# Kernel optimization log

Hardware: AMD Instinct MI355X
Metric: run time of the kernel (lower is better)

## Reference

```python
import jax, jax.numpy as jnp
import numpy as np

N_NODES = 100000
N_EDGES = 2000000
EPS = 1e-8


def setup_inputs() -> dict:
    key = jax.random.key(0)
    k1, k2 = jax.random.split(key)
    node_positions = jax.random.normal(k1, (1, N_NODES, 2), dtype=jnp.float32) * 10.0
    adjacency = jnp.zeros((1, 1, 1), dtype=jnp.float32)  # unused by this axiom
    edge_index = jax.random.randint(k2, (2, N_EDGES), 0, N_NODES, dtype=jnp.int32)
    return {"node_positions": node_positions, "adjacency": adjacency, "edge_index": edge_index}


def reference(node_positions, adjacency, edge_index):
    """OrthogonalIntegrityAxiom loss.

    Mathematically identical to enumerating all intra-node edge pairs (i<j)
    and averaging cos^2(theta)*(1-cos^2(theta)) = dot^2 - dot^4 over pairs.
    Uses the moment identity: per node n with incident unit directions d_i,
      sum_{i,j} (d_i.d_j)^2 = ||sum_i d_i (x) d_i||_F^2
      sum_{i,j} (d_i.d_j)^4 = ||sum_i d_i^{(x)4}||_F^2
    Diagonal (i=j) terms equal 1 in both sums and cancel in the difference,
    so sum_{i<j} (dot^2 - dot^4) = (S2_n - S4_n)/2.
    """
    pos = node_positions.reshape(-1, 2)                      # (N, 2)
    n_total = pos.shape[0]
    src, dst = edge_index[0], edge_index[1]
    d = pos[dst] - pos[src]                                  # (E, 2)
    d = d / jnp.maximum(jnp.linalg.norm(d, axis=-1, keepdims=True), EPS)

    # Each edge is incident to both endpoints -> 2E (node, direction) pairs.
    nodes = jnp.concatenate([src, dst])                      # (2E,)
    dirs = jnp.concatenate([d, d], axis=0)                   # (2E, 2)

    o2 = (dirs[:, :, None] * dirs[:, None, :]).reshape(-1, 4)    # d (x) d, (2E, 4)
    o4 = (o2[:, :, None] * o2[:, None, :]).reshape(-1, 16)       # d^{(x)4}, (2E, 16)

    M = jax.ops.segment_sum(o2, nodes, num_segments=n_total)     # (N, 4)
    T = jax.ops.segment_sum(o4, nodes, num_segments=n_total)     # (N, 16)
    deg = jax.ops.segment_sum(jnp.ones_like(dirs[:, 0]), nodes, num_segments=n_total)

    S2 = jnp.sum(M * M, axis=-1)   # per-node sum_{i,j} (d_i.d_j)^2
    S4 = jnp.sum(T * T, axis=-1)   # per-node sum_{i,j} (d_i.d_j)^4

    pair_loss_sum = 0.5 * jnp.sum(S2 - S4)
    n_pairs = 0.5 * jnp.sum(deg * (deg - 1.0))
    loss = pair_loss_sum / jnp.maximum(n_pairs, 1.0)
    return loss
```

## Files before the change

kernel.cpp:

```cpp
#include <hip/hip_runtime.h>
#include <math.h>

#define EPSV 1e-8f

static constexpr double QC = 1.0 / 1024.0;
static constexpr double QS = 1.0 / 512.0;

static constexpr int BLOG = 8;
static constexpr int NPB = 1 << BLOG;
static constexpr int NBIN = 512;
static constexpr int SRTN = 8192;
static constexpr int NREP = 8;
static constexpr int NODE_BLOCKS = 256;

__device__ __forceinline__ unsigned int make_record(float dx, float dy) {
    float n2 = dx * dx + dy * dy;
    if (n2 > EPSV * EPSV) {
        float inv = 1.0f / n2;
        float c2 = (dx * dx - dy * dy) * inv;
        float s2 = (2.0f * dx * dy) * inv;
        float c4 = c2 * c2 - s2 * s2;
        float s4 = 2.0f * c2 * s2;
        c4 = fminf(fmaxf(c4, -1.0f), 1.0f);
        s4 = fminf(fmaxf(s4, -1.0f), 1.0f);
        unsigned int c4q = (unsigned int)__float2int_rn((c4 + 1.0f) * 1024.0f);
        unsigned int s4q = (unsigned int)__float2int_rn((s4 + 1.0f) * 512.0f);
        return (c4q << 11) | s4q;
    }
    return (1u << 31) | (1024u << 11) | 512u;
}

__device__ __forceinline__ unsigned long long rec_to_val(unsigned int r) {
    return (((unsigned long long)(r >> 31)) << 60) | (1ull << 52)
         | (((unsigned long long)((r >> 11) & 0xFFFu)) << 26)
         | (unsigned long long)(r & 0x7FFu);
}

__device__ __forceinline__ void decode_accum(unsigned long long a, double& pls, double& npr) {
    double s4sum = (double)(a & 0x3FFFFFFull);
    double c4sum = (double)((a >> 26) & 0x3FFFFFFull);
    double deg = (double)((a >> 52) & 0xFFull);
    double z = (double)(a >> 60);
    double u = deg - z;
    double C = c4sum * QC - deg;
    double S = s4sum * QS - deg;
    pls += (u * u - C * C - S * S) * 0.0625;
    npr += 0.5 * deg * (deg - 1.0);
}

__global__ __launch_bounds__(256) void bin_kernel(
    const float2* __restrict__ pos,
    const int* __restrict__ ei,
    int E, int NB, int chunk, int rstride,
    unsigned short* __restrict__ ofs,
    unsigned int* __restrict__ buf)
{
    __shared__ unsigned int srt[SRTN];
    __shared__ unsigned int hist[512];
    __shared__ unsigned int scan[512];
    int blk = blockIdx.x;
    int t = threadIdx.x;
    int e0 = blk * chunk;
    int e1 = min(E, e0 + chunk);
    const int* src = ei;
    const int* dst = ei + E;

    hist[t] = 0; hist[t + 256] = 0;
    __syncthreads();
    for (int e = e0 + t; e < e1; e += 256) {
        atomicAdd(&hist[src[e] >> BLOG], 1u);
        atomicAdd(&hist[dst[e] >> BLOG], 1u);
    }
    __syncthreads();
    scan[t] = hist[t]; scan[t + 256] = hist[t + 256];
    __syncthreads();
    for (int d = 1; d < 512; d <<= 1) {
        unsigned a0 = scan[t] + ((t >= d) ? scan[t - d] : 0u);
        int t2 = t + 256;
        unsigned a1 = scan[t2] + ((t2 >= d) ? scan[t2 - d] : 0u);
        __syncthreads();
        scan[t] = a0; scan[t2] = a1;
        __syncthreads();
    }
    unsigned ex0 = scan[t] - hist[t];
    unsigned ex1 = scan[t + 256] - hist[t + 256];
    if (t <= NB) ofs[(size_t)t * NBIN + blk] = (unsigned short)ex0;
    if (t + 256 <= NB) ofs[(size_t)(t + 256) * NBIN + blk] = (unsigned short)ex1;
    __syncthreads();
    hist[t] = ex0; hist[t + 256] = ex1;
    __syncthreads();
    for (int e = e0 + t; e < e1; e += 256) {
        int s = src[e], d = dst[e];
        float2 ps = pos[s], pd = pos[d];
        unsigned int rec = make_record(pd.x - ps.x, pd.y - ps.y);
        unsigned is = atomicAdd(&hist[s >> BLOG], 1u);
        srt[is] = rec | ((unsigned)(s & (NPB - 1)) << 23);
        unsigned it = atomicAdd(&hist[d >> BLOG], 1u);
        srt[it] = rec | ((unsigned)(d & (NPB - 1)) << 23);
    }
    __syncthreads();
    int nrec = 2 * max(0, e1 - e0);
    unsigned int* db = buf + (size_t)blk * (size_t)rstride;
    int nv = nrec >> 2;
    const uint4* s4 = (const uint4*)srt;
    uint4* d4 = (uint4*)db;
    for (int i = t; i < nv; i += 256) d4[i] = s4[i];
    for (int i = (nv << 2) + t; i < nrec; i += 256) db[i] = srt[i];
}

__global__ __launch_bounds__(1024) void bucket_kernel(
    const unsigned int* __restrict__ buf,
    const unsigned short* __restrict__ ofs,
    int rstride,
    double* __restrict__ partials)
{
    __shared__ unsigned long long acc[NREP][NPB];
    __shared__ unsigned short o0s[NBIN];
    __shared__ unsigned int sc[NBIN + 1];
    __shared__ double sha[16], shb[16];
    int b = blockIdx.x;
    int t = threadIdx.x;
    int wid = t >> 6;
    for (int i = t; i < NREP * NPB; i += 1024)
        ((unsigned long long*)acc)[i] = 0ull;
    if (t < NBIN) {
        unsigned o0 = ofs[(size_t)b * NBIN + t];
        unsigned o1 = ofs[(size_t)(b + 1) * NBIN + t];
        o0s[t] = (unsigned short)o0;
        sc[t + 1] = o1 - o0;
    }
    if (t == 0) sc[0] = 0;
    __syncthreads();
    for (int d = 1; d < NBIN; d <<= 1) {
        unsigned v = 0;
        if (t < NBIN) v = sc[t + 1] + ((t + 1 > d) ? sc[t + 1 - d] : 0u);
        __syncthreads();
        if (t < NBIN) sc[t + 1] = v;
        __syncthreads();
    }
    int cnt = sc[NBIN];

    int rep = wid & (NREP - 1);
    for (int idx = t; idx < cnt; idx += 1024) {
        int lo = 0, hi = NBIN;
        while (hi - lo > 1) {
            int mid = (lo + hi) >> 1;
            if ((unsigned)idx >= sc[mid]) lo = mid; else hi = mid;
        }
        unsigned r = buf[(size_t)lo * (size_t)rstride + o0s[lo] + (unsigned)idx - sc[lo]];
        atomicAdd(&acc[rep][(r >> 23) & (NPB - 1)], rec_to_val(r));
    }
    __syncthreads();

    double pls = 0.0, npr = 0.0;
    for (int i = t; i < NPB; i += 1024) {
        unsigned long long a = 0;
        for (int rr = 0; rr < NREP; ++rr) a += acc[rr][i];
        decode_accum(a, pls, npr);
    }
    for (int off = 32; off > 0; off >>= 1) {
        pls += __shfl_down(pls, off, 64);
        npr += __shfl_down(npr, off, 64);
    }
    if ((t & 63) == 0) { sha[wid] = pls; shb[wid] = npr; }
    __syncthreads();
    if (t == 0) {
        double a = 0.0, bb = 0.0;
        for (int i = 0; i < 16; ++i) { a += sha[i]; bb += shb[i]; }
        partials[2 * b + 0] = a;
        partials[2 * b + 1] = bb;
    }
}

__global__ __launch_bounds__(256) void final_kernel(
    const double* __restrict__ partials,
    float* __restrict__ out,
    int nb)
{
    double pls = 0.0, npr = 0.0;
    for (int i = threadIdx.x; i < nb; i += blockDim.x) {
        pls += partials[2 * i + 0];
        npr += partials[2 * i + 1];
    }
    __shared__ double sha[4], shb[4];
    for (int off = 32; off > 0; off >>= 1) {
        pls += __shfl_down(pls, off, 64);
        npr += __shfl_down(npr, off, 64);
    }
    int lane = threadIdx.x & 63;
    int wid = threadIdx.x >> 6;
    if (lane == 0) { sha[wid] = pls; shb[wid] = npr; }
    __syncthreads();
    if (threadIdx.x == 0) {
        double a = sha[0] + sha[1] + sha[2] + sha[3];
        double b = shb[0] + shb[1] + shb[2] + shb[3];
        out[0] = (float)(a / fmax(b, 1.0));
    }
}

__global__ __launch_bounds__(256) void edge_kernel_fb(
    const float2* __restrict__ pos,
    const int* __restrict__ ei,
    unsigned long long* __restrict__ acc,
    int E)
{
    int tid = blockIdx.x * blockDim.x + threadIdx.x;
    int nthreads = gridDim.x * blockDim.x;
    const int* src = ei;
    const int* dst = ei + E;
    for (int e = tid; e < E; e += nthreads) {
        int s = src[e], t = dst[e];
        float2 ps = pos[s], pt = pos[t];
        unsigned long long val = rec_to_val(make_record(pt.x - ps.x, pt.y - ps.y));
        atomicAdd(&acc[s], val);
        atomicAdd(&acc[t], val);
    }
}

__global__ __launch_bounds__(256) void node_kernel_fb(
    const unsigned long long* __restrict__ acc,
    double* __restrict__ partials,
    int N)
{
    int tid = blockIdx.x * blockDim.x + threadIdx.x;
    int nthreads = gridDim.x * blockDim.x;
    double pls = 0.0, npr = 0.0;
    for (int n = tid; n < N; n += nthreads)
        decode_accum(acc[n], pls, npr);
    __shared__ double sha[4], shb[4];
    for (int off = 32; off > 0; off >>= 1) {
        pls += __shfl_down(pls, off, 64);
        npr += __shfl_down(npr, off, 64);
    }
    int lane = threadIdx.x & 63;
    int wid = threadIdx.x >> 6;
    if (lane == 0) { sha[wid] = pls; shb[wid] = npr; }
    __syncthreads();
    if (threadIdx.x == 0) {
        partials[2 * blockIdx.x + 0] = sha[0] + sha[1] + sha[2] + sha[3];
        partials[2 * blockIdx.x + 1] = shb[0] + shb[1] + shb[2] + shb[3];
    }
}

extern "C" void kernel_launch(void* const* d_in, const int* in_sizes, int n_in,
                              void* d_out, int out_size, void* d_ws, size_t ws_size,
                              hipStream_t stream) {
    const float* pos = (const float*)d_in[0];
    const int* ei = (const int*)d_in[2];
    int N = in_sizes[0] / 2;
    int E = in_sizes[2] / 2;
    float* out = (float*)d_out;

    int NB = (N + NPB - 1) >> BLOG;
    int chunk = (E + NBIN - 1) / NBIN;
    int nrec_max = 2 * chunk;
    int rstride = (nrec_max + 15) & ~15;

    size_t off_buf = (size_t)NB * 16;
    size_t off_ofs = off_buf + (size_t)NBIN * (size_t)rstride * 4;
    size_t need = off_ofs + (size_t)(NB + 1) * (size_t)NBIN * 2;

    if (ws_size >= need && nrec_max <= SRTN && NB + 1 <= 512 && nrec_max < 65536) {
        double* partials = (double*)d_ws;
        unsigned int* buf = (unsigned int*)((char*)d_ws + off_buf);
        unsigned short* ofs = (unsigned short*)((char*)d_ws + off_ofs);

        bin_kernel<<<NBIN, 256, 0, stream>>>(
            (const float2*)pos, ei, E, NB, chunk, rstride, ofs, buf);
        bucket_kernel<<<NB, 1024, 0, stream>>>(buf, ofs, rstride, partials);
        final_kernel<<<1, 256, 0, stream>>>(partials, out, NB);
    } else {
        unsigned long long* acc = (unsigned long long*)d_ws;
        double* partials = (double*)((char*)d_ws + (size_t)N * 8);
        hipMemsetAsync(d_ws, 0, (size_t)N * 8 + (size_t)NODE_BLOCKS * 16, stream);
        int eb = min((E + 255) / 256, 2048);
        edge_kernel_fb<<<eb, 256, 0, stream>>>((const float2*)pos, ei, acc, E);
        node_kernel_fb<<<NODE_BLOCKS, 256, 0, stream>>>(acc, partials, N);
        final_kernel<<<1, 256, 0, stream>>>(partials, out, NODE_BLOCKS);
    }
}
```

Before: 117.2 us.

## Scatter bins directly to global and fuse final reduction via atomics

The binning kernel now writes sorted records straight to the global buffer instead of staging them in a 32KB shared array and copying out, and it runs 512 threads per block. The separate final reduction kernel is removed: each bucket block atomically adds its partial sums into a global accumulator, and the last block to finish computes the output. This removes a launch and the shared staging copy, at the cost of uncoalesced global scatter writes and a nondeterministic floating-point summation order.

New measurement: 133.7 us. 14.1% more time.

```diff
diff --git a/kernel.cpp b/kernel.cpp
--- a/kernel.cpp
+++ b/kernel.cpp
@@ -9,7 +9,6 @@
 static constexpr int BLOG = 8;
 static constexpr int NPB = 1 << BLOG;
 static constexpr int NBIN = 512;
-static constexpr int SRTN = 8192;
 static constexpr int NREP = 8;
 static constexpr int NODE_BLOCKS = 256;
 
@@ -48,14 +47,15 @@
     npr += 0.5 * deg * (deg - 1.0);
 }
 
-__global__ __launch_bounds__(256) void bin_kernel(
+
+__global__ __launch_bounds__(512) void bin_kernel(
     const float2* __restrict__ pos,
     const int* __restrict__ ei,
     int E, int NB, int chunk, int rstride,
     unsigned short* __restrict__ ofs,
-    unsigned int* __restrict__ buf)
-{
-    __shared__ unsigned int srt[SRTN];
+    unsigned int* __restrict__ buf,
+    unsigned long long* __restrict__ g_tail)
+{
     __shared__ unsigned int hist[512];
     __shared__ unsigned int scan[512];
     int blk = blockIdx.x;
@@ -65,54 +65,46 @@
     const int* src = ei;
     const int* dst = ei + E;
 
-    hist[t] = 0; hist[t + 256] = 0;
-    __syncthreads();
-    for (int e = e0 + t; e < e1; e += 256) {
+    if (blk == 0 && t < 3) g_tail[t] = 0ull;
+
+    hist[t] = 0;
+    __syncthreads();
+    for (int e = e0 + t; e < e1; e += 512) {
         atomicAdd(&hist[src[e] >> BLOG], 1u);
         atomicAdd(&hist[dst[e] >> BLOG], 1u);
     }
     __syncthreads();
-    scan[t] = hist[t]; scan[t + 256] = hist[t + 256];
+    scan[t] = hist[t];
     __syncthreads();
     for (int d = 1; d < 512; d <<= 1) {
-        unsigned a0 = scan[t] + ((t >= d) ? scan[t - d] : 0u);
-        int t2 = t + 256;
-        unsigned a1 = scan[t2] + ((t2 >= d) ? scan[t2 - d] : 0u);
-        __syncthreads();
-        scan[t] = a0; scan[t2] = a1;
-        __syncthreads();
-    }
-    unsigned ex0 = scan[t] - hist[t];
-    unsigned ex1 = scan[t + 256] - hist[t + 256];
-    if (t <= NB) ofs[(size_t)t * NBIN + blk] = (unsigned short)ex0;
-    if (t + 256 <= NB) ofs[(size_t)(t + 256) * NBIN + blk] = (unsigned short)ex1;
-    __syncthreads();
-    hist[t] = ex0; hist[t + 256] = ex1;
-    __syncthreads();
-    for (int e = e0 + t; e < e1; e += 256) {
+        unsigned v = scan[t] + ((t >= d) ? scan[t - d] : 0u);
+        __syncthreads();
+        scan[t] = v;
+        __syncthreads();
+    }
+    unsigned ex = scan[t] - hist[t];
+    if (t <= NB) ofs[(size_t)t * NBIN + blk] = (unsigned short)ex;
+    __syncthreads();
+    hist[t] = ex;
+    __syncthreads();
+    unsigned int* db = buf + (size_t)blk * (size_t)rstride;
+    for (int e = e0 + t; e < e1; e += 512) {
         int s = src[e], d = dst[e];
         float2 ps = pos[s], pd = pos[d];
         unsigned int rec = make_record(pd.x - ps.x, pd.y - ps.y);
         unsigned is = atomicAdd(&hist[s >> BLOG], 1u);
-        srt[is] = rec | ((unsigned)(s & (NPB - 1)) << 23);
+        db[is] = rec | ((unsigned)(s & (NPB - 1)) << 23);
         unsigned it = atomicAdd(&hist[d >> BLOG], 1u);
-        srt[it] = rec | ((unsigned)(d & (NPB - 1)) << 23);
-    }
-    __syncthreads();
-    int nrec = 2 * max(0, e1 - e0);
-    unsigned int* db = buf + (size_t)blk * (size_t)rstride;
-    int nv = nrec >> 2;
-    const uint4* s4 = (const uint4*)srt;
-    uint4* d4 = (uint4*)db;
-    for (int i = t; i < nv; i += 256) d4[i] = s4[i];
-    for (int i = (nv << 2) + t; i < nrec; i += 256) db[i] = srt[i];
+        db[it] = rec | ((unsigned)(d & (NPB - 1)) << 23);
+    }
 }
 
 __global__ __launch_bounds__(1024) void bucket_kernel(
     const unsigned int* __restrict__ buf,
     const unsigned short* __restrict__ ofs,
     int rstride,
-    double* __restrict__ partials)
+    unsigned long long* __restrict__ g_tail,
+    float* __restrict__ out)
 {
     __shared__ unsigned long long acc[NREP][NPB];
     __shared__ unsigned short o0s[NBIN];
@@ -167,34 +159,17 @@
     if (t == 0) {
         double a = 0.0, bb = 0.0;
         for (int i = 0; i < 16; ++i) { a += sha[i]; bb += shb[i]; }
-        partials[2 * b + 0] = a;
-        partials[2 * b + 1] = bb;
-    }
-}
-
-__global__ __launch_bounds__(256) void final_kernel(
-    const double* __restrict__ partials,
-    float* __restrict__ out,
-    int nb)
-{
-    double pls = 0.0, npr = 0.0;
-    for (int i = threadIdx.x; i < nb; i += blockDim.x) {
-        pls += partials[2 * i + 0];
-        npr += partials[2 * i + 1];
-    }
-    __shared__ double sha[4], shb[4];
-    for (int off = 32; off > 0; off >>= 1) {
-        pls += __shfl_down(pls, off, 64);
-        npr += __shfl_down(npr, off, 64);
-    }
-    int lane = threadIdx.x & 63;
-    int wid = threadIdx.x >> 6;
-    if (lane == 0) { sha[wid] = pls; shb[wid] = npr; }
-    __syncthreads();
-    if (threadIdx.x == 0) {
-        double a = sha[0] + sha[1] + sha[2] + sha[3];
-        double b = shb[0] + shb[1] + shb[2] + shb[3];
-        out[0] = (float)(a / fmax(b, 1.0));
+        double* gacc = (double*)g_tail;
+        atomicAdd(&gacc[0], a);
+        atomicAdd(&gacc[1], bb);
+        __threadfence();
+        unsigned long long done = atomicAdd(&g_tail[2], 1ull);
+        if (done == (unsigned long long)gridDim.x - 1) {
+            __threadfence();
+            double fa = __hip_atomic_load(&gacc[0], __ATOMIC_RELAXED, __HIP_MEMORY_SCOPE_AGENT);
+            double fb = __hip_atomic_load(&gacc[1], __ATOMIC_RELAXED, __HIP_MEMORY_SCOPE_AGENT);
+            out[0] = (float)(fa / fmax(fb, 1.0));
+        }
     }
 }
 
@@ -242,6 +217,32 @@
     }
 }
 
+__global__ __launch_bounds__(256) void final_kernel_fb(
+    const double* __restrict__ partials,
+    float* __restrict__ out,
+    int nb)
+{
+    double pls = 0.0, npr = 0.0;
+    for (int i = threadIdx.x; i < nb; i += blockDim.x) {
+        pls += partials[2 * i + 0];
+        npr += partials[2 * i + 1];
+    }
+    __shared__ double sha[4], shb[4];
+    for (int off = 32; off > 0; off >>= 1) {
+        pls += __shfl_down(pls, off, 64);
+        npr += __shfl_down(npr, off, 64);
+    }
+    int lane = threadIdx.x & 63;
+    int wid = threadIdx.x >> 6;
+    if (lane == 0) { sha[wid] = pls; shb[wid] = npr; }
+    __syncthreads();
+    if (threadIdx.x == 0) {
+        double a = sha[0] + sha[1] + sha[2] + sha[3];
+        double b = shb[0] + shb[1] + shb[2] + shb[3];
+        out[0] = (float)(a / fmax(b, 1.0));
+    }
+}
+
 extern "C" void kernel_launch(void* const* d_in, const int* in_sizes, int n_in,
                               void* d_out, int out_size, void* d_ws, size_t ws_size,
                               hipStream_t stream) {
@@ -256,19 +257,19 @@
     int nrec_max = 2 * chunk;
     int rstride = (nrec_max + 15) & ~15;
 
-    size_t off_buf = (size_t)NB * 16;
-    size_t off_ofs = off_buf + (size_t)NBIN * (size_t)rstride * 4;
-    size_t need = off_ofs + (size_t)(NB + 1) * (size_t)NBIN * 2;
-
-    if (ws_size >= need && nrec_max <= SRTN && NB + 1 <= 512 && nrec_max < 65536) {
-        double* partials = (double*)d_ws;
+    size_t off_ofs = 64;
+    size_t ofs_bytes = ((size_t)(NB + 1) * NBIN * 2 + 63) & ~(size_t)63;
+    size_t off_buf = off_ofs + ofs_bytes;
+    size_t need = off_buf + (size_t)NBIN * (size_t)rstride * 4;
+
+    if (ws_size >= need && NB + 1 <= 512 && nrec_max < 65536) {
+        unsigned long long* g_tail = (unsigned long long*)d_ws;
+        unsigned short* ofs = (unsigned short*)((char*)d_ws + off_ofs);
         unsigned int* buf = (unsigned int*)((char*)d_ws + off_buf);
-        unsigned short* ofs = (unsigned short*)((char*)d_ws + off_ofs);
-
-        bin_kernel<<<NBIN, 256, 0, stream>>>(
-            (const float2*)pos, ei, E, NB, chunk, rstride, ofs, buf);
-        bucket_kernel<<<NB, 1024, 0, stream>>>(buf, ofs, rstride, partials);
-        final_kernel<<<1, 256, 0, stream>>>(partials, out, NB);
+
+        bin_kernel<<<NBIN, 512, 0, stream>>>(
+            (const float2*)pos, ei, E, NB, chunk, rstride, ofs, buf, g_tail);
+        bucket_kernel<<<NB, 1024, 0, stream>>>(buf, ofs, rstride, g_tail, out);
     } else {
         unsigned long long* acc = (unsigned long long*)d_ws;
         double* partials = (double*)((char*)d_ws + (size_t)N * 8);
@@ -276,6 +277,6 @@
         int eb = min((E + 255) / 256, 2048);
         edge_kernel_fb<<<eb, 256, 0, stream>>>((const float2*)pos, ei, acc, E);
         node_kernel_fb<<<NODE_BLOCKS, 256, 0, stream>>>(acc, partials, N);
-        final_kernel<<<1, 256, 0, stream>>>(partials, out, NODE_BLOCKS);
-    }
-}
+        final_kernel_fb<<<1, 256, 0, stream>>>(partials, out, NODE_BLOCKS);
+    }
+}
```
